# Optimization experiments

Measured on AMD Instinct MI355X. Metric: run time of the kernel, lower is better.

The kernel has to match this reference:

```python
import jax, jax.numpy as jnp
import numpy as np

N_EMBD = 768
N_HEAD = 12
BLOCK_SIZE = 1024


def setup_inputs() -> dict:
    key = jax.random.key(0)
    ks = jax.random.split(key, 11)
    s = lambda fan_in: 1.0 / np.sqrt(fan_in)
    x = jax.random.normal(ks[0], (8, 1024, N_EMBD), dtype=jnp.float32)
    return {
        "x": x,
        "ln1_g": jnp.ones((N_EMBD,), jnp.float32),
        "ln1_b": jnp.zeros((N_EMBD,), jnp.float32),
        "w_attn": jax.random.normal(ks[1], (N_EMBD, 3 * N_EMBD), jnp.float32) * s(N_EMBD),
        "b_attn": jnp.zeros((3 * N_EMBD,), jnp.float32),
        "w_proj": jax.random.normal(ks[2], (N_EMBD, N_EMBD), jnp.float32) * s(N_EMBD),
        "b_proj": jnp.zeros((N_EMBD,), jnp.float32),
        "ln2_g": jnp.ones((N_EMBD,), jnp.float32),
        "ln2_b": jnp.zeros((N_EMBD,), jnp.float32),
        "w_fc": jax.random.normal(ks[3], (N_EMBD, 4 * N_EMBD), jnp.float32) * s(N_EMBD),
        "b_fc": jnp.zeros((4 * N_EMBD,), jnp.float32),
        "w_fc_proj": jax.random.normal(ks[4], (4 * N_EMBD, N_EMBD), jnp.float32) * s(4 * N_EMBD),
        "b_fc_proj": jnp.zeros((N_EMBD,), jnp.float32),
    }


def _layernorm(x, g, b, eps=1e-5):
    mu = jnp.mean(x, axis=-1, keepdims=True)
    var = jnp.var(x, axis=-1, keepdims=True)
    return (x - mu) * jax.lax.rsqrt(var + eps) * g + b


def _gelu_tanh(x):
    # GELU with tanh approximation (matches nn.GELU(approximate='tanh'))
    c = np.sqrt(2.0 / np.pi).astype(np.float32)
    return 0.5 * x * (1.0 + jnp.tanh(c * (x + 0.044715 * x * x * x)))


def _attn(x, w_attn, b_attn, w_proj, b_proj):
    B, T, C = x.shape
    hs = C // N_HEAD
    qkv = x @ w_attn + b_attn  # [B,T,3C]
    q, k, v = jnp.split(qkv, 3, axis=-1)
    # [B,T,C] -> [B,nh,T,hs]
    to_heads = lambda t: t.reshape(B, T, N_HEAD, hs).transpose(0, 2, 1, 3)
    q, k, v = to_heads(q), to_heads(k), to_heads(v)
    att = jnp.einsum('bhqd,bhkd->bhqk', q, k) * (1.0 / np.sqrt(hs))
    causal = jnp.tril(jnp.ones((T, T), bool))
    att = jnp.where(causal, att, -jnp.inf)
    att = jax.nn.softmax(att, axis=-1)
    y = jnp.einsum('bhqk,bhkd->bhqd', att, v)  # [B,nh,T,hs]
    y = y.transpose(0, 2, 1, 3).reshape(B, T, C)
    return y @ w_proj + b_proj


def reference(x, ln1_g, ln1_b, w_attn, b_attn, w_proj, b_proj,
              ln2_g, ln2_b, w_fc, b_fc, w_fc_proj, b_fc_proj):
    x = x + _attn(_layernorm(x, ln1_g, ln1_b), w_attn, b_attn, w_proj, b_proj)
    h = _layernorm(x, ln2_g, ln2_b)
    h = _gelu_tanh(h @ w_fc + b_fc) @ w_fc_proj + b_fc_proj
    return x + h
```

## Files before the change

kernel.cpp:

```cpp
#include <hip/hip_runtime.h>

typedef __bf16 bf16x8 __attribute__((ext_vector_type(8)));
typedef float  f32x4  __attribute__((ext_vector_type(4)));
typedef unsigned short ushort8 __attribute__((ext_vector_type(8)));

__device__ __forceinline__ unsigned short f2bf(float f) {
    unsigned u = __float_as_uint(f);
    u += 0x7FFFu + ((u >> 16) & 1u);
    return (unsigned short)(u >> 16);
}

__device__ __forceinline__ f32x4 mfma16x16x32(bf16x8 a, bf16x8 b, f32x4 c) {
    return __builtin_amdgcn_mfma_f32_16x16x32_bf16(a, b, c, 0, 0, 0);
}

__device__ __forceinline__ bf16x8 ld8(const unsigned short* p) {
    return __builtin_bit_cast(bf16x8, *(const ushort8*)p);
}

__device__ __forceinline__ float exp2_fast(float x) {
    float r; asm("v_exp_f32 %0, %1" : "=v"(r) : "v"(x)); return r;
}

__device__ __forceinline__ void glds16(const unsigned short* g, unsigned short* l) {
    __builtin_amdgcn_global_load_lds(
        (const __attribute__((address_space(1))) void*)g,
        (__attribute__((address_space(3))) void*)l, 16, 0, 0);
}

__device__ __forceinline__ float gelu_tanh(float x) {
    const float c = 0.7978845608028654f;
    float z = c * (x + 0.044715f * x * x * x);
    float e = __expf(2.f * z);
    float th = 1.f - 2.f / (e + 1.f);
    return 0.5f * x * (1.f + th);
}

#define N_EMBD 768
#define SEQ    1024
#define NHEAD  12
#define HS     64
#define MROWS  8192

__global__ __launch_bounds__(256) void tcast_kernel(const float* __restrict__ in,
                                                    unsigned short* __restrict__ out,
                                                    int K, int N) {
    __shared__ float tile[32][33];
    int nb = blockIdx.x * 32, kb = blockIdx.y * 32;
    int tx = threadIdx.x, ty = threadIdx.y;
#pragma unroll
    for (int i = 0; i < 4; i++) {
        int k = kb + ty + i * 8;
        tile[ty + i * 8][tx] = in[(size_t)k * N + nb + tx];
    }
    __syncthreads();
#pragma unroll
    for (int i = 0; i < 4; i++) {
        int n = nb + ty + i * 8;
        out[(size_t)n * K + kb + tx] = f2bf(tile[tx][ty + i * 8]);
    }
}

__global__ __launch_bounds__(256) void ln_kernel(const float* __restrict__ x,
                                                 const float* __restrict__ g,
                                                 const float* __restrict__ b,
                                                 unsigned short* __restrict__ out) {
    int row = blockIdx.x;
    const float* xr = x + (size_t)row * N_EMBD;
    float v[3], s = 0.f, s2 = 0.f;
#pragma unroll
    for (int i = 0; i < 3; i++) {
        v[i] = xr[threadIdx.x + i * 256];
        s += v[i]; s2 += v[i] * v[i];
    }
#pragma unroll
    for (int m = 1; m < 64; m <<= 1) { s += __shfl_xor(s, m); s2 += __shfl_xor(s2, m); }
    __shared__ float ps[4], ps2[4];
    int wid = threadIdx.x >> 6;
    if ((threadIdx.x & 63) == 0) { ps[wid] = s; ps2[wid] = s2; }
    __syncthreads();
    s  = ps[0] + ps[1] + ps[2] + ps[3];
    s2 = ps2[0] + ps2[1] + ps2[2] + ps2[3];
    float mu  = s * (1.f / N_EMBD);
    float var = s2 * (1.f / N_EMBD) - mu * mu;
    float inv = rsqrtf(var + 1e-5f);
#pragma unroll
    for (int i = 0; i < 3; i++) {
        int c = threadIdx.x + i * 256;
        out[(size_t)row * N_EMBD + c] = f2bf((v[i] - mu) * inv * g[c] + b[c]);
    }
}

template <int EPI, int WM>
__global__ __launch_bounds__(256) void gemm_bt_kernel(
    const unsigned short* __restrict__ A, const unsigned short* __restrict__ BT,
    const float* __restrict__ bias, const float* __restrict__ res,
    float* __restrict__ outF, unsigned short* __restrict__ outB,
    int M, int N, int K) {
    constexpr int BM = WM * 32;
    __shared__ __attribute__((aligned(16))) unsigned short As[BM * 64];
    __shared__ __attribute__((aligned(16))) unsigned short Bs[128 * 64];
    const int gx = gridDim.x;
    const int slot = blockIdx.y * gx + blockIdx.x;
    const int chunk = (gx * gridDim.y) >> 3;
    const int logical = (slot & 7) * chunk + (slot >> 3);
    const int m0 = (logical / gx) * BM, n0 = (logical % gx) * 128;
    const int t = threadIdx.x, lane = t & 63, wid = t >> 6;
    const int wr = wid >> 1, wc = wid & 1;

    f32x4 acc[WM][4] = {};

    const int rrow = lane & 15, g = lane >> 4;
    const int swz8 = (rrow & 7) << 3;

    const int srow = t >> 3;
    const int scol = ((t & 7) ^ (srow & 7)) * 8;

    for (int kk = 0; kk < K; kk += 64) {
#pragma unroll
        for (int i = 0; i < WM; i++)
            glds16(&A[(size_t)(m0 + i * 32 + srow) * K + kk + scol], &As[i * 2048 + wid * 512]);
#pragma unroll
        for (int i = 0; i < 4; i++)
            glds16(&BT[(size_t)(n0 + i * 32 + srow) * K + kk + scol], &Bs[i * 2048 + wid * 512]);
        __syncthreads();
#pragma unroll
        for (int s = 0; s < 2; s++) {
            bf16x8 af[WM], bfr[4];
#pragma unroll
            for (int i = 0; i < WM; i++) {
                int row = wr * (WM * 16) + i * 16 + rrow;
                af[i] = ld8(&As[row * 64 + ((((s << 2) | g) << 3) ^ swz8)]);
            }
#pragma unroll
            for (int j = 0; j < 4; j++) {
                int row = wc * 64 + j * 16 + rrow;
                bfr[j] = ld8(&Bs[row * 64 + ((((s << 2) | g) << 3) ^ swz8)]);
            }
#pragma unroll
            for (int i = 0; i < WM; i++)
#pragma unroll
                for (int j = 0; j < 4; j++) acc[i][j] = mfma16x16x32(af[i], bfr[j], acc[i][j]);
        }
        __syncthreads();
    }

    const int crow = g * 4, ccol = rrow;
#pragma unroll
    for (int i = 0; i < WM; i++) {
        int gr0 = m0 + wr * (WM * 16) + i * 16 + crow;
#pragma unroll
        for (int j = 0; j < 4; j++) {
            int gc = n0 + wc * 64 + j * 16 + ccol;
            float bv = bias[gc];
#pragma unroll
            for (int r = 0; r < 4; r++) {
                int gr = gr0 + r;
                float v = acc[i][j][r] + bv;
                if constexpr (EPI == 1) v = gelu_tanh(v);
                if constexpr (EPI == 2) {
                    outF[(size_t)gr * N + gc] = v + res[(size_t)gr * N + gc];
                } else {
                    outB[(size_t)gr * N + gc] = f2bf(v);
                }
            }
        }
    }
}

#define SCALE_LOG2E 0.18033688011112042f
#define DEFER_TH    11.5f

__device__ __forceinline__ void attn_tile(
    const unsigned short* Ks, const unsigned short* Vt, unsigned short* P,
    const bf16x8* qf, f32x4* yacc, float* mrow, float* lrow,
    int q0w, int kv0, bool masked, int lane)
{
    const int rrow = lane & 15, g = lane >> 4, kg8 = g * 8;
    f32x4 s[4];
#pragma unroll
    for (int ct = 0; ct < 4; ct++) {
        const int j = ct * 16 + rrow;
        const unsigned short* kr = &Ks[j * 64];
        f32x4 z = {};
        z = mfma16x16x32(qf[0], ld8(&kr[((g    ) ^ (j & 7)) * 8]), z);
        z = mfma16x16x32(qf[1], ld8(&kr[((g + 4) ^ (j & 7)) * 8]), z);
        s[ct] = z;
    }
    float pmax[4] = {-1e30f, -1e30f, -1e30f, -1e30f};
    const int qrb = q0w + g * 4;
#pragma unroll
    for (int ct = 0; ct < 4; ct++) {
        const int j = kv0 + ct * 16 + rrow;
#pragma unroll
        for (int r = 0; r < 4; r++) {
            float v = s[ct][r] * SCALE_LOG2E;
            if (masked && j > qrb + r) v = -1e30f;
            s[ct][r] = v;
            pmax[r] = fmaxf(pmax[r], v);
        }
    }
#pragma unroll
    for (int m = 1; m < 16; m <<= 1)
#pragma unroll
        for (int r = 0; r < 4; r++) pmax[r] = fmaxf(pmax[r], __shfl_xor(pmax[r], m));
    bool need = false;
#pragma unroll
    for (int r = 0; r < 4; r++) need |= (pmax[r] > mrow[r] + DEFER_TH);
    if (__any(need)) {
#pragma unroll
        for (int r = 0; r < 4; r++) {
            float mn = fmaxf(mrow[r], pmax[r]);
            float a = exp2_fast(mrow[r] - mn);
            mrow[r] = mn;
            lrow[r] *= a;
#pragma unroll
            for (int dt = 0; dt < 4; dt++) yacc[dt][r] *= a;
        }
    }
#pragma unroll
    for (int ct = 0; ct < 4; ct++)
#pragma unroll
        for (int r = 0; r < 4; r++) {
            const int q = g * 4 + r;
            P[q * 80 + ((ct * 16 + rrow) ^ ((q & 7) << 3))] = f2bf(exp2_fast(s[ct][r] - mrow[r]));
        }
    asm volatile("s_waitcnt lgkmcnt(0)" ::: "memory");
    const int sw = (rrow & 7) << 3;
    bf16x8 pa0 = ld8(&P[rrow * 80 + ((kg8     ) ^ sw)]);
    bf16x8 pa1 = ld8(&P[rrow * 80 + ((kg8 + 32) ^ sw)]);
    const bf16x8 vones = __builtin_bit_cast(bf16x8,
        (ushort8){0x3F80, 0x3F80, 0x3F80, 0x3F80, 0x3F80, 0x3F80, 0x3F80, 0x3F80});
    f32x4 ss = {};
    ss = mfma16x16x32(pa0, vones, ss);
    ss = mfma16x16x32(pa1, vones, ss);
#pragma unroll
    for (int r = 0; r < 4; r++) lrow[r] += ss[r];
#pragma unroll
    for (int dt = 0; dt < 4; dt++) {
        const unsigned short* vr = &Vt[(dt * 16 + rrow) * 88];
        yacc[dt] = mfma16x16x32(pa0, ld8(&vr[kg8     ]), yacc[dt]);
        yacc[dt] = mfma16x16x32(pa1, ld8(&vr[kg8 + 32]), yacc[dt]);
    }
}

__global__ __launch_bounds__(512, 6) void attn_kernel(const unsigned short* __restrict__ qkv,
                                                      unsigned short* __restrict__ yb) {
    const int slot = blockIdx.y * 8 + blockIdx.x;
    const int logical = (slot & 7) * 96 + (slot >> 3);
    const int p = logical & 7;
    const int bh = logical >> 3;
    const int b = bh / NHEAD, h = bh % NHEAD;
    const int t = threadIdx.x, lane = t & 63, wid = t >> 6;
    const int half = wid >> 2, w4 = wid & 3;
    const int qt = half ? p : (15 - p);
    const int ntSelf = half ? (p + 1) : (16 - p);
    const int ntMax = 16 - p;
    const int q0w = qt * 64 + w4 * 16;
    const int rrow = lane & 15, g = lane >> 4, kg8 = g * 8;

    __shared__ __attribute__((aligned(16))) unsigned short Ks[64 * 64];
    __shared__ __attribute__((aligned(16))) unsigned short Vt[64 * 88];
    __shared__ __attribute__((aligned(16))) unsigned short Ps[8][16 * 80];

    bf16x8 qf[2];
    {
        size_t base = ((size_t)(b * SEQ + q0w + rrow)) * 2304 + h * HS;
        qf[0] = ld8(&qkv[base + kg8]);
        qf[1] = ld8(&qkv[base + 32 + kg8]);
    }

    f32x4 y[4] = {};
    float mrow[4], lrow[4];
#pragma unroll
    for (int r = 0; r < 4; r++) { mrow[r] = -1e30f; lrow[r] = 0.f; }

    const int kr0 = t >> 3;
    const int kc0 = ((t & 7) ^ (kr0 & 7)) * 8;
    const int vd = t & 63, vk = (t >> 6) * 8;

    for (int tt = 0; tt < ntMax; tt++) {
        const int kv0 = tt * 64;
        __syncthreads();
        glds16(&qkv[((size_t)(b * SEQ + kv0 + kr0)) * 2304 + 768 + h * HS + kc0], &Ks[wid * 512]);
        ushort8 v8;
#pragma unroll
        for (int i = 0; i < 8; i++)
            v8[i] = qkv[((size_t)(b * SEQ + kv0 + vk + i)) * 2304 + 1536 + h * HS + vd];
        *(ushort8*)&Vt[vd * 88 + vk] = v8;
        __syncthreads();

        if (tt < ntSelf)
            attn_tile(Ks, Vt, &Ps[wid][0], qf, y, mrow, lrow, q0w, kv0, tt == ntSelf - 1, lane);
    }

#pragma unroll
    for (int dt = 0; dt < 4; dt++)
#pragma unroll
        for (int r = 0; r < 4; r++) {
            int col = h * HS + dt * 16 + rrow;
            yb[((size_t)(b * SEQ + q0w + g * 4 + r)) * N_EMBD + col] = f2bf(y[dt][r] / lrow[r]);
        }
}

extern "C" void kernel_launch(void* const* d_in, const int* in_sizes, int n_in,
                              void* d_out, int out_size, void* d_ws, size_t ws_size,
                              hipStream_t stream) {
    const float* x        = (const float*)d_in[0];
    const float* ln1_g    = (const float*)d_in[1];
    const float* ln1_b    = (const float*)d_in[2];
    const float* w_attn   = (const float*)d_in[3];
    const float* b_attn   = (const float*)d_in[4];
    const float* w_proj   = (const float*)d_in[5];
    const float* b_proj   = (const float*)d_in[6];
    const float* ln2_g    = (const float*)d_in[7];
    const float* ln2_b    = (const float*)d_in[8];
    const float* w_fc     = (const float*)d_in[9];
    const float* b_fc     = (const float*)d_in[10];
    const float* w_fcp    = (const float*)d_in[11];
    const float* b_fcp    = (const float*)d_in[12];
    float* out = (float*)d_out;

    unsigned short* ws = (unsigned short*)d_ws;
    unsigned short* wT_attn = ws;
    unsigned short* wT_proj = wT_attn + 2304 * 768;
    unsigned short* wT_fc   = wT_proj + 768 * 768;
    unsigned short* wT_fcp  = wT_fc   + 3072 * 768;
    unsigned short* xb      = wT_fcp  + 768 * 3072;
    unsigned short* qkv     = xb      + (size_t)MROWS * 768;
    unsigned short* yb      = qkv     + (size_t)MROWS * 2304;
    unsigned short* act     = qkv;
    float* x2 = (float*)(yb + (size_t)MROWS * 768);

    dim3 tb(32, 8);
    tcast_kernel<<<dim3(2304 / 32, 768 / 32), tb, 0, stream>>>(w_attn, wT_attn, 768, 2304);
    tcast_kernel<<<dim3(768 / 32, 768 / 32),  tb, 0, stream>>>(w_proj, wT_proj, 768, 768);
    tcast_kernel<<<dim3(3072 / 32, 768 / 32), tb, 0, stream>>>(w_fc,   wT_fc,   768, 3072);
    tcast_kernel<<<dim3(768 / 32, 3072 / 32), tb, 0, stream>>>(w_fcp,  wT_fcp,  3072, 768);

    ln_kernel<<<MROWS, 256, 0, stream>>>(x, ln1_g, ln1_b, xb);
    gemm_bt_kernel<0, 4><<<dim3(2304 / 128, MROWS / 128), 256, 0, stream>>>(
        xb, wT_attn, b_attn, nullptr, nullptr, qkv, MROWS, 2304, 768);
    attn_kernel<<<dim3(8, 96), 512, 0, stream>>>(qkv, yb);
    gemm_bt_kernel<2, 2><<<dim3(768 / 128, MROWS / 64), 256, 0, stream>>>(
        yb, wT_proj, b_proj, x, x2, nullptr, MROWS, 768, 768);
    ln_kernel<<<MROWS, 256, 0, stream>>>(x2, ln2_g, ln2_b, xb);
    gemm_bt_kernel<1, 4><<<dim3(3072 / 128, MROWS / 128), 256, 0, stream>>>(
        xb, wT_fc, b_fc, nullptr, nullptr, act, MROWS, 3072, 768);
    gemm_bt_kernel<2, 2><<<dim3(768 / 128, MROWS / 64), 256, 0, stream>>>(
        act, wT_fcp, b_fcp, x2, out, nullptr, MROWS, 768, 3072);
}
```

Before: 294.0 us.

## Prefetch next K/V tile into registers during attention compute

The attention loop now loads the next K and V tile from global memory into registers while the current tile is being computed. At the top of each iteration it stores them to LDS, replacing the direct global-to-LDS K load and the synchronous V gather. Explicit waitcnt, sched_barrier and s_barrier calls take the place of __syncthreads, and a sched_barrier is added after the P-store wait in the tile routine. The aim is to hide global load latency behind the MFMA work, at the cost of more registers and a vmcnt(0) wait that may still stall.

```diff
diff --git a/kernel.cpp b/kernel.cpp
--- a/kernel.cpp
+++ b/kernel.cpp
@@ -226,6 +226,7 @@
             P[q * 80 + ((ct * 16 + rrow) ^ ((q & 7) << 3))] = f2bf(exp2_fast(s[ct][r] - mrow[r]));
         }
     asm volatile("s_waitcnt lgkmcnt(0)" ::: "memory");
+    __builtin_amdgcn_sched_barrier(0);
     const int sw = (rrow & 7) << 3;
     bf16x8 pa0 = ld8(&P[rrow * 80 + ((kg8     ) ^ sw)]);
     bf16x8 pa1 = ld8(&P[rrow * 80 + ((kg8 + 32) ^ sw)]);
@@ -276,22 +277,37 @@
     for (int r = 0; r < 4; r++) { mrow[r] = -1e30f; lrow[r] = 0.f; }
 
     const int kr0 = t >> 3;
-    const int kc0 = ((t & 7) ^ (kr0 & 7)) * 8;
+    const size_t kgoff = (size_t)kr0 * 2304 + 768 + h * HS + (t & 7) * 8;
+    const int kdst = kr0 * 64 + (((t & 7) ^ (kr0 & 7)) * 8);
     const int vd = t & 63, vk = (t >> 6) * 8;
+    const size_t vgoff = (size_t)vk * 2304 + 1536 + h * HS + vd;
+    const int vdst = vd * 88 + vk;
+    const unsigned short* kvbase = qkv + (size_t)(b * SEQ) * 2304;
+
+    ushort8 kregA, vregA, kregB = {}, vregB = {};
+    kregA = *(const ushort8*)&kvbase[kgoff];
+#pragma unroll
+    for (int i = 0; i < 8; i++) vregA[i] = kvbase[vgoff + (size_t)i * 2304];
 
     for (int tt = 0; tt < ntMax; tt++) {
-        const int kv0 = tt * 64;
-        __syncthreads();
-        glds16(&qkv[((size_t)(b * SEQ + kv0 + kr0)) * 2304 + 768 + h * HS + kc0], &Ks[wid * 512]);
-        ushort8 v8;
-#pragma unroll
-        for (int i = 0; i < 8; i++)
-            v8[i] = qkv[((size_t)(b * SEQ + kv0 + vk + i)) * 2304 + 1536 + h * HS + vd];
-        *(ushort8*)&Vt[vd * 88 + vk] = v8;
-        __syncthreads();
-
+        asm volatile("s_waitcnt vmcnt(0)" ::: "memory");
+        __builtin_amdgcn_sched_barrier(0);
+        __builtin_amdgcn_s_barrier();
+        *(ushort8*)&Ks[kdst] = kregA;
+        *(ushort8*)&Vt[vdst] = vregA;
+        if (tt + 1 < ntMax) {
+            const size_t off = (size_t)(tt + 1) * 64 * 2304;
+            kregB = *(const ushort8*)&kvbase[off + kgoff];
+#pragma unroll
+            for (int i = 0; i < 8; i++) vregB[i] = kvbase[off + vgoff + (size_t)i * 2304];
+        }
+        asm volatile("s_waitcnt lgkmcnt(0)" ::: "memory");
+        __builtin_amdgcn_sched_barrier(0);
+        __builtin_amdgcn_s_barrier();
         if (tt < ntSelf)
-            attn_tile(Ks, Vt, &Ps[wid][0], qf, y, mrow, lrow, q0w, kv0, tt == ntSelf - 1, lane);
+            attn_tile(Ks, Vt, &Ps[wid][0], qf, y, mrow, lrow, q0w, tt * 64,
+                      tt == ntSelf - 1, lane);
+        kregA = kregB; vregA = vregB;
     }
 
 #pragma unroll
```

Result: slower. 333.1 us (+13.3%).

## Double-buffer GEMM shared-memory tiles to overlap global loads with MFMA

Applied to the files above, without the earlier changes.

Turns the bf16 GEMM main loop into a two-stage pipeline. The next K-tile is loaded into an alternate LDS buffer while the current tile is consumed by MFMAs, which hides global-load latency behind compute. LDS usage doubles, which may cut occupancy. Correctness depends on glds16 being async and on the single barrier per iteration ordering the buffer reuse. A scheduling barrier is also added in the attention kernel after the P-store wait, so the compiler cannot move the P reads ahead of it.

```diff
diff --git a/kernel.cpp b/kernel.cpp
--- a/kernel.cpp
+++ b/kernel.cpp
@@ -98,8 +98,10 @@
     float* __restrict__ outF, unsigned short* __restrict__ outB,
     int M, int N, int K) {
     constexpr int BM = WM * 32;
-    __shared__ __attribute__((aligned(16))) unsigned short As[BM * 64];
-    __shared__ __attribute__((aligned(16))) unsigned short Bs[128 * 64];
+    constexpr int ASZ = BM * 64;
+    constexpr int BSZ = 128 * 64;
+    __shared__ __attribute__((aligned(16))) unsigned short As[2 * ASZ];
+    __shared__ __attribute__((aligned(16))) unsigned short Bs[2 * BSZ];
     const int gx = gridDim.x;
     const int slot = blockIdx.y * gx + blockIdx.x;
     const int chunk = (gx * gridDim.y) >> 3;
@@ -116,26 +118,43 @@
     const int srow = t >> 3;
     const int scol = ((t & 7) ^ (srow & 7)) * 8;
 
-    for (int kk = 0; kk < K; kk += 64) {
-#pragma unroll
-        for (int i = 0; i < WM; i++)
-            glds16(&A[(size_t)(m0 + i * 32 + srow) * K + kk + scol], &As[i * 2048 + wid * 512]);
-#pragma unroll
-        for (int i = 0; i < 4; i++)
-            glds16(&BT[(size_t)(n0 + i * 32 + srow) * K + kk + scol], &Bs[i * 2048 + wid * 512]);
-        __syncthreads();
+    const int NT = K >> 6;
+#pragma unroll
+    for (int i = 0; i < WM; i++)
+        glds16(&A[(size_t)(m0 + i * 32 + srow) * K + scol], &As[i * 2048 + wid * 512]);
+#pragma unroll
+    for (int i = 0; i < 4; i++)
+        glds16(&BT[(size_t)(n0 + i * 32 + srow) * K + scol], &Bs[i * 2048 + wid * 512]);
+    __syncthreads();
+
+    int cur = 0;
+    for (int kt = 0; kt < NT; ++kt) {
+        if (kt + 1 < NT) {
+            const int kk = (kt + 1) << 6;
+            const int nb = (cur ^ 1);
+#pragma unroll
+            for (int i = 0; i < WM; i++)
+                glds16(&A[(size_t)(m0 + i * 32 + srow) * K + kk + scol],
+                       &As[nb * ASZ + i * 2048 + wid * 512]);
+#pragma unroll
+            for (int i = 0; i < 4; i++)
+                glds16(&BT[(size_t)(n0 + i * 32 + srow) * K + kk + scol],
+                       &Bs[nb * BSZ + i * 2048 + wid * 512]);
+        }
+        const unsigned short* ab = &As[cur * ASZ];
+        const unsigned short* bb = &Bs[cur * BSZ];
 #pragma unroll
         for (int s = 0; s < 2; s++) {
             bf16x8 af[WM], bfr[4];
 #pragma unroll
             for (int i = 0; i < WM; i++) {
                 int row = wr * (WM * 16) + i * 16 + rrow;
-                af[i] = ld8(&As[row * 64 + ((((s << 2) | g) << 3) ^ swz8)]);
+                af[i] = ld8(&ab[row * 64 + ((((s << 2) | g) << 3) ^ swz8)]);
             }
 #pragma unroll
             for (int j = 0; j < 4; j++) {
                 int row = wc * 64 + j * 16 + rrow;
-                bfr[j] = ld8(&Bs[row * 64 + ((((s << 2) | g) << 3) ^ swz8)]);
+                bfr[j] = ld8(&bb[row * 64 + ((((s << 2) | g) << 3) ^ swz8)]);
             }
 #pragma unroll
             for (int i = 0; i < WM; i++)
@@ -143,6 +162,7 @@
                 for (int j = 0; j < 4; j++) acc[i][j] = mfma16x16x32(af[i], bfr[j], acc[i][j]);
         }
         __syncthreads();
+        cur ^= 1;
     }
 
     const int crow = g * 4, ccol = rrow;
@@ -226,6 +246,7 @@
             P[q * 80 + ((ct * 16 + rrow) ^ ((q & 7) << 3))] = f2bf(exp2_fast(s[ct][r] - mrow[r]));
         }
     asm volatile("s_waitcnt lgkmcnt(0)" ::: "memory");
+    __builtin_amdgcn_sched_barrier(0);
     const int sw = (rrow & 7) << 3;
     bf16x8 pa0 = ld8(&P[rrow * 80 + ((kg8     ) ^ sw)]);
     bf16x8 pa1 = ld8(&P[rrow * 80 + ((kg8 + 32) ^ sw)]);
```

Result: faster. 285.2 us (-3.0%).
